# Performance work log

Hardware: AMD Instinct MI355X
Metric: run time of the kernel (lower is better)

The kernel has to match this reference:

```python
import jax, jax.numpy as jnp
import numpy as np

N = 16384      # tokens
D_IN = 256     # input feature dim
D = 1024       # d_model
H = 2048       # expert hidden dim (2 * d_model)
E = 8          # n_experts
K = 2          # top_k
OUT = 2        # output classes
EPS = 1e-5


def layernorm(x, g, b):
    m = jnp.mean(x, axis=-1, keepdims=True)
    v = jnp.mean(jnp.square(x - m), axis=-1, keepdims=True)
    return (x - m) * jax.lax.rsqrt(v + EPS) * g + b


def setup_inputs() -> dict:
    key = jax.random.key(0)
    ks = jax.random.split(key, 10)
    s_in = 1.0 / np.sqrt(D_IN)
    s_d = 1.0 / np.sqrt(D)
    s_h = 1.0 / np.sqrt(H)
    return {
        "x": jax.random.normal(ks[0], (N, D_IN), jnp.float32),
        "w_in": jax.random.normal(ks[1], (D_IN, D), jnp.float32) * s_in,
        "b_in": jnp.zeros((D,), jnp.float32),
        "g_in": jnp.ones((D,), jnp.float32),
        "beta_in": jnp.zeros((D,), jnp.float32),
        "w_gate": jax.random.normal(ks[2], (D, E), jnp.float32) * s_d,
        "w1": jax.random.normal(ks[3], (E, D, H), jnp.float32) * s_d,
        "b1": jnp.zeros((E, H), jnp.float32),
        "w2": jax.random.normal(ks[4], (E, H, D), jnp.float32) * s_h,
        "b2": jnp.zeros((E, D), jnp.float32),
        "g_moe": jnp.ones((D,), jnp.float32),
        "beta_moe": jnp.zeros((D,), jnp.float32),
        "g_out": jnp.ones((D,), jnp.float32),
        "beta_out": jnp.zeros((D,), jnp.float32),
        "w_cls": jax.random.normal(ks[5], (D, OUT), jnp.float32) * s_d,
        "b_cls": jnp.zeros((OUT,), jnp.float32),
    }


def reference(x, w_in, b_in, g_in, beta_in, w_gate, w1, b1, w2, b2,
              g_moe, beta_moe, g_out, beta_out, w_cls, b_cls):
    # input projection + norm
    h = layernorm(x @ w_in + b_in, g_in, beta_in)            # [N, D]
    # router: softmax then top-k, renormalize over selected experts
    probs = jax.nn.softmax(h @ w_gate, axis=-1)              # [N, E]
    _, top_idx = jax.lax.top_k(probs, K)                     # [N, K]
    sel = jax.nn.one_hot(top_idx, E, dtype=probs.dtype).sum(axis=1)  # [N, E] 0/1
    gates = probs * sel
    gates = gates / (jnp.sum(gates, axis=-1, keepdims=True) + 1e-9)
    # experts: weighted combine; gate==0 tokens contribute nothing (same math
    # as the torch masked gather/scatter-add, dropout off in eval)
    mixed = jnp.zeros_like(h)
    for e in range(E):  # fixed, small expert count
        expert_out = jax.nn.gelu(h @ w1[e] + b1[e]) @ w2[e] + b2[e]  # [N, D]
        mixed = mixed + gates[:, e:e + 1] * expert_out
    out = layernorm(h + mixed, g_moe, beta_moe)
    out = layernorm(out, g_out, beta_out)
    return out @ w_cls + b_cls                               # [N, OUT]
```

## Files before the change

kernel.cpp:

```cpp
#include <hip/hip_runtime.h>
#include <hip/hip_bf16.h>

#define D_IN 256
#define DM   1024
#define HD   2048
#define NE   8
#define NTOK 16384

typedef __attribute__((ext_vector_type(8))) short short8;
typedef __attribute__((ext_vector_type(4))) float f32x4;
typedef unsigned int uint;

#define MT_TOFF1 0
#define MT_TOFF2 512
#define MT_CNT1  1536
#define MT_P1    1600
#define MT_OFF1  1664
#define MT_CNT2  1728
#define MT_PCNT2 1856
#define MT_TOTAL 1984

__device__ inline ushort f2bf(float v){
  __hip_bfloat16 b = __float2bfloat16(v);
  return *reinterpret_cast<ushort*>(&b);
}
__device__ inline float bf2f(ushort u){
  __hip_bfloat16 b = *reinterpret_cast<__hip_bfloat16*>(&u);
  return __bfloat162float(b);
}

__device__ inline float gelu_tanh(float x){
  float x3 = x*x*x;
  float t = tanhf(0.7978845608028654f*(x + 0.044715f*x3));
  return 0.5f*x*(1.0f+t);
}

__device__ inline void gload16(const void* g, void* l){
  __builtin_amdgcn_global_load_lds(
      (const __attribute__((address_space(1))) void*)g,
      (__attribute__((address_space(3))) void*)l, 16, 0, 0);
}

__global__ __launch_bounds__(256) void transpose_bf16_kernel(
    const float* __restrict__ src, ushort* __restrict__ dst, int R, int C)
{
  __shared__ float tile[32][33];
  int e = blockIdx.z;
  src += (size_t)e*R*C; dst += (size_t)e*R*C;
  int c0 = blockIdx.x*32, r0 = blockIdx.y*32;
  int tx = threadIdx.x & 31, ty = threadIdx.x >> 5;
  #pragma unroll
  for (int rr = ty; rr < 32; rr += 8)
    tile[rr][tx] = src[(size_t)(r0+rr)*C + c0+tx];
  __syncthreads();
  #pragma unroll
  for (int rr = ty; rr < 32; rr += 8)
    dst[(size_t)(c0+rr)*R + r0+tx] = f2bf(tile[tx][rr]);
}

__global__ __launch_bounds__(256) void split_x_kernel(
    const float* __restrict__ x, ushort* __restrict__ xs3)
{
  int g = blockIdx.x*256 + threadIdx.x;
  int e0 = g*4;
  int row = e0 >> 8, col = e0 & 255;
  f32x4 v = *(const f32x4*)(x + (size_t)row*D_IN + col);
  ushort4 hi, mi, lo;
  #pragma unroll
  for (int i=0;i<4;++i){
    float f = v[i];
    ushort h = f2bf(f);       float fh = bf2f(h);
    ushort m = f2bf(f - fh);  float fm = bf2f(m);
    ushort l = f2bf(f - fh - fm);
    ((ushort*)&hi)[i]=h; ((ushort*)&mi)[i]=m; ((ushort*)&lo)[i]=l;
  }
  ushort* base = xs3 + (size_t)row*768 + col;
  *(ushort4*)(base)       = hi;
  *(ushort4*)(base + 256) = mi;
  *(ushort4*)(base + 512) = lo;
}

__global__ __launch_bounds__(256) void transpose_split3_kernel(
    const float* __restrict__ src, ushort* __restrict__ dst)
{
  __shared__ float tile[32][33];
  int c0 = blockIdx.x*32, r0 = blockIdx.y*32;
  int tx = threadIdx.x & 31, ty = threadIdx.x >> 5;
  #pragma unroll
  for (int rr = ty; rr < 32; rr += 8)
    tile[rr][tx] = src[(size_t)(r0+rr)*DM + c0+tx];
  __syncthreads();
  #pragma unroll
  for (int rr = ty; rr < 32; rr += 8){
    float f = tile[tx][rr];
    ushort h = f2bf(f);       float fh = bf2f(h);
    ushort m = f2bf(f - fh);  float fm = bf2f(m);
    ushort l = f2bf(f - fh - fm);
    ushort* d = dst + (size_t)(c0+rr)*768 + r0 + tx;
    d[0]   = h;
    d[256] = m;
    d[512] = l;
  }
}

__global__ __launch_bounds__(256) void wgate_t_kernel(
    const float* __restrict__ w_gate, float* __restrict__ wgt)
{
  int e = blockIdx.x;
  for (int j = threadIdx.x; j < DM; j += 256)
    wgt[(size_t)e*DM + j] = w_gate[(size_t)j*NE + e];
}

__global__ __launch_bounds__(256) void gemm_router(
    const ushort* __restrict__ A,
    const ushort* __restrict__ BT,
    const float* __restrict__ b_in,
    float* __restrict__ y)
{
  __shared__ ushort As[128*32];
  __shared__ ushort Bs[128*32];
  const int tid = threadIdx.x;
  const int w = tid>>6, l = tid&63;
  const int wm = w>>1, wn = w&1;
  const int bm0 = blockIdx.y*128, bn0 = blockIdx.x*128;
  const int lr = l&15, lk = l>>4;
  const int rsub = l>>2, csub = (l&3)*8;

  const ushort* ag[2]; const ushort* bg[2];
  ushort* al[2]; ushort* bl[2];
  #pragma unroll
  for (int i=0;i<2;++i){
    int ra = bm0 + w*32 + i*16 + rsub;
    int rb = bn0 + w*32 + i*16 + rsub;
    ag[i] = A  + (size_t)ra*768 + csub;
    bg[i] = BT + (size_t)rb*768 + csub;
    al[i] = (ushort*)As + (w*32 + i*16)*32;
    bl[i] = (ushort*)Bs + (w*32 + i*16)*32;
  }

  f32x4 zero = {0.f,0.f,0.f,0.f};
  f32x4 acc[4][4];
  #pragma unroll
  for (int i=0;i<4;++i){
    #pragma unroll
    for (int j=0;j<4;++j) acc[i][j]=zero;
  }

  const int pq[6][2] = {{0,0},{256,0},{0,256},{256,256},{512,0},{0,512}};
  for (int t=0;t<6;++t){
    int pOff = pq[t][0], qOff = pq[t][1];
    for (int kt=0; kt<256; kt+=32){
      #pragma unroll
      for (int i=0;i<2;++i){
        gload16(ag[i]+pOff+kt, al[i]);
        gload16(bg[i]+qOff+kt, bl[i]);
      }
      __syncthreads();
      short8 af[4], bf[4];
      #pragma unroll
      for (int i=0;i<4;++i) af[i] = *(const short8*)(As + (wm*64 + i*16 + lr)*32 + lk*8);
      #pragma unroll
      for (int j=0;j<4;++j) bf[j] = *(const short8*)(Bs + (wn*64 + j*16 + lr)*32 + lk*8);
      #pragma unroll
      for (int i=0;i<4;++i){
        #pragma unroll
        for (int j=0;j<4;++j)
          acc[i][j] = __builtin_amdgcn_mfma_f32_16x16x32_bf16(af[i], bf[j], acc[i][j], 0, 0, 0);
      }
      __syncthreads();
    }
  }

  #pragma unroll
  for (int i=0;i<4;++i){
    #pragma unroll
    for (int j=0;j<4;++j){
      int n = bn0 + wn*64 + j*16 + lr;
      float bn_ = b_in[n];
      #pragma unroll
      for (int r=0;r<4;++r){
        int m = bm0 + wm*64 + i*16 + lk*4 + r;
        y[(size_t)m*DM + n] = acc[i][j][r] + bn_;
      }
    }
  }
}

__device__ inline double wredd(double v){
  #pragma unroll
  for (int o=32;o>0;o>>=1) v += __shfl_xor(v, o, 64);
  return v;
}

__global__ __launch_bounds__(256) void ln_router_kernel(
    const float* __restrict__ g_in, const float* __restrict__ beta_in,
    const float* __restrict__ wgt,
    ushort* __restrict__ hbf, float* __restrict__ resid,
    float* __restrict__ gates, int* __restrict__ selmask)
{
  int tok = blockIdx.x*4 + (threadIdx.x>>6);
  int l = threadIdx.x & 63;
  float* row = resid + (size_t)tok*DM;
  float u[16];
  double s=0.0, q=0.0;
  #pragma unroll
  for (int r=0;r<16;++r){ u[r]=row[l+64*r]; s+=u[r]; q+=(double)u[r]*u[r]; }
  s = wredd(s); q = wredd(q);
  double mean = s*(1.0/1024.0);
  double var  = q*(1.0/1024.0) - mean*mean;
  double rstd = 1.0/sqrt(var + 1e-5);

  double lg[NE];
  #pragma unroll
  for (int e=0;e<NE;++e) lg[e]=0.0;
  float hv[16];
  #pragma unroll
  for (int r=0;r<16;++r){
    int j = l + 64*r;
    double v = ((double)u[r]-mean)*rstd*(double)g_in[j] + (double)beta_in[j];
    hv[r] = (float)v;
    #pragma unroll
    for (int e=0;e<NE;++e) lg[e] += v*(double)wgt[(size_t)e*DM + j];
  }
  #pragma unroll
  for (int r=0;r<16;++r){
    int j = l + 64*r;
    row[j] = hv[r];
    hbf[(size_t)tok*DM + j] = f2bf(hv[r]);
  }
  #pragma unroll
  for (int e=0;e<NE;++e) lg[e] = wredd(lg[e]);

  if (l==0){
    double mx = lg[0];
    #pragma unroll
    for (int e=1;e<NE;++e) mx = lg[e]>mx ? lg[e] : mx;
    double p[NE]; double sum=0.0;
    #pragma unroll
    for (int e=0;e<NE;++e){ p[e]=exp(lg[e]-mx); sum+=p[e]; }
    #pragma unroll
    for (int e=0;e<NE;++e) p[e]/=sum;
    int i1=0;
    for (int e=1;e<NE;++e) if (p[e]>p[i1]) i1=e;
    int i2=-1;
    for (int e=0;e<NE;++e){ if (e==i1) continue; if (i2<0 || p[e]>p[i2]) i2=e; }
    double denom = p[i1]+p[i2]+1e-9;
    float g[NE];
    #pragma unroll
    for (int e=0;e<NE;++e) g[e]=0.f;
    g[i1]=(float)(p[i1]/denom);
    g[i2]=(float)(p[i2]/denom);
    #pragma unroll
    for (int e=0;e<NE;++e) gates[(size_t)tok*NE+e]=g[e];
    selmask[tok] = (1<<i1)|(1<<i2);
  }
}

__global__ __launch_bounds__(256) void builder_count(
    const int* __restrict__ selmask, uint* __restrict__ bc1, uint* __restrict__ bc2)
{
  __shared__ uint c1[8], c2s[16];
  int b = blockIdx.x, tid = threadIdx.x;
  if (tid<8) c1[tid]=0;
  if (tid<16) c2s[tid]=0;
  __syncthreads();
  int m = selmask[b*256+tid];
  int ea = __ffs(m)-1, eb = 31-__clz(m);
  atomicAdd(&c1[ea],1u); atomicAdd(&c1[eb],1u);
  atomicAdd(&c2s[ea],1u); atomicAdd(&c2s[8+eb],1u);
  __syncthreads();
  if (tid<8) bc1[b*8+tid]=c1[tid];
  if (tid<16) bc2[b*16+tid]=c2s[tid];
}

__global__ __launch_bounds__(256) void builder_scan(
    const uint* __restrict__ bc1, const uint* __restrict__ bc2,
    uint* __restrict__ meta, int nch, int TPC)
{
  int tid = threadIdx.x;
  int c = tid/24, k = tid%24;
  if (c < nch){
    if (k < 8){
      uint run=0;
      for (int b=c*TPC; b<(c+1)*TPC; ++b){ meta[MT_TOFF1 + b*8 + k] = run; run += bc1[b*8+k]; }
      meta[MT_CNT1 + c*8 + k] = run;
    } else {
      int k2 = k-8;
      uint run=0;
      for (int b=c*TPC; b<(c+1)*TPC; ++b){ meta[MT_TOFF2 + b*16 + k2] = run; run += bc2[b*16+k2]; }
      meta[MT_CNT2 + c*16 + k2] = run;
      meta[MT_PCNT2 + c*16 + k2] = ((run + 127u)/128u)*128u;
    }
  }
  __syncthreads();
  if (tid < nch){
    uint off=0;
    for (int e=0;e<8;++e){
      uint cn = meta[MT_CNT1 + tid*8 + e];
      uint p = ((cn+127u)/128u)*128u;
      meta[MT_P1 + tid*8 + e] = p;
      meta[MT_OFF1 + tid*8 + e] = off;
      off += p;
    }
  }
}

__device__ inline int exclscan256(int v, int* sc, int tid){
  sc[tid]=v; __syncthreads();
  #pragma unroll
  for (int o=1;o<256;o<<=1){
    int x = (tid>=o) ? sc[tid-o] : 0;
    __syncthreads();
    sc[tid]+=x;
    __syncthreads();
  }
  int incl = sc[tid]; __syncthreads();
  return incl - v;
}

__global__ __launch_bounds__(256) void builder_fill(
    const int* __restrict__ selmask, const uint* __restrict__ meta,
    int* __restrict__ ids1, int* __restrict__ g2row, int* __restrict__ g2tok,
    int CH)
{
  __shared__ int sc[256];
  int b = blockIdx.x, tid = threadIdx.x;
  int t = b*256 + tid;
  int c = t / CH;
  int m = selmask[t];
  int ea = __ffs(m)-1, eb = 31-__clz(m);
  int ja=0, jb=0;
  for (int e=0;e<8;++e){
    int r0 = exclscan256((ea==e)?1:0, sc, tid);
    if (ea==e) ja = r0;
    int r1 = exclscan256((eb==e)?1:0, sc, tid);
    if (eb==e) jb = r1;
  }
  {
    uint j    = meta[MT_TOFF2 + b*16 + ea] + (uint)ja;
    uint pos1 = j;
    uint row  = meta[MT_OFF1 + c*8 + ea] + pos1;
    ids1[(c*8+ea)*CH + pos1] = t;
    g2row[((c*2+0)*8+ea)*CH + j] = (int)row;
    g2tok[((c*2+0)*8+ea)*CH + j] = t;
  }
  {
    uint j    = meta[MT_TOFF2 + b*16 + 8 + eb] + (uint)jb;
    uint pos1 = meta[MT_CNT2 + c*16 + eb] + j;
    uint row  = meta[MT_OFF1 + c*8 + eb] + pos1;
    ids1[(c*8+eb)*CH + pos1] = t;
    g2row[((c*2+1)*8+eb)*CH + j] = (int)row;
    g2tok[((c*2+1)*8+eb)*CH + j] = t;
  }
}

template<int EPI>
__global__ __launch_bounds__(256) void gemm_sparse(
    const ushort* __restrict__ Abase,
    const ushort* __restrict__ BT,
    const int*   __restrict__ rows,
    const int*   __restrict__ toks,
    const uint*  __restrict__ pcnt,
    const uint*  __restrict__ cnt,
    const uint*  __restrict__ off1,
    const float* __restrict__ bias,
    const float* __restrict__ gates,
    ushort* __restrict__ t1,
    float*  __restrict__ resid,
    int K, int N, int CH)
{
  const int e = blockIdx.z;
  const int bm0 = blockIdx.y*128;
  if ((uint)bm0 >= pcnt[e]) return;
  const int bn0 = blockIdx.x*128;

  __shared__ ushort As[128*32];
  __shared__ ushort Bs[128*32];
  const int tid = threadIdx.x;
  const int w = tid>>6, l = tid&63;
  const int wm = w>>1, wn = w&1;
  const int lr = l&15, lk = l>>4;
  const int rsub = l>>2, csub = (l&3)*8;

  const ushort* ag[2]; const ushort* bg[2];
  ushort* al[2]; ushort* bl[2];
  #pragma unroll
  for (int i=0;i<2;++i){
    int ra = w*32 + i*16 + rsub;
    int id = rows[e*CH + bm0 + ra];
    ag[i] = Abase + (size_t)id*K + csub;
    int rb = bn0 + w*32 + i*16 + rsub;
    bg[i] = BT + (size_t)e*N*K + (size_t)rb*K + csub;
    al[i] = (ushort*)As + (w*32 + i*16)*32;
    bl[i] = (ushort*)Bs + (w*32 + i*16)*32;
  }

  f32x4 zero = {0.f,0.f,0.f,0.f};
  f32x4 acc[4][4];
  #pragma unroll
  for (int i=0;i<4;++i){
    #pragma unroll
    for (int j=0;j<4;++j) acc[i][j]=zero;
  }

  for (int kt = 0; kt < K; kt += 32) {
    #pragma unroll
    for (int i=0;i<2;++i){
      gload16(ag[i]+kt, al[i]);
      gload16(bg[i]+kt, bl[i]);
    }
    __syncthreads();
    short8 af[4], bf[4];
    #pragma unroll
    for (int i=0;i<4;++i) af[i] = *(const short8*)(As + (wm*64 + i*16 + lr)*32 + lk*8);
    #pragma unroll
    for (int j=0;j<4;++j) bf[j] = *(const short8*)(Bs + (wn*64 + j*16 + lr)*32 + lk*8);
    #pragma unroll
    for (int i=0;i<4;++i){
      #pragma unroll
      for (int j=0;j<4;++j)
        acc[i][j] = __builtin_amdgcn_mfma_f32_16x16x32_bf16(af[i], bf[j], acc[i][j], 0, 0, 0);
    }
    __syncthreads();
  }

  #pragma unroll
  for (int i=0;i<4;++i){
    #pragma unroll
    for (int j=0;j<4;++j){
      int n = bn0 + wn*64 + j*16 + lr;
      float bn_ = bias[(size_t)e*N + n];
      #pragma unroll
      for (int r=0;r<4;++r){
        int mloc = wm*64 + i*16 + lk*4 + r;
        float v = acc[i][j][r] + bn_;
        if (EPI==0){
          size_t trow = (size_t)off1[e] + bm0 + mloc;
          t1[trow*N + n] = f2bf(gelu_tanh(v));
        } else {
          int mg = bm0 + mloc;
          if ((uint)mg < cnt[e]){
            int tok = toks[e*CH + mg];
            float g = gates[(size_t)tok*NE + e];
            resid[(size_t)tok*N + n] += g*v;
          }
        }
      }
    }
  }
}

__global__ __launch_bounds__(64) void final_kernel(
    const float* __restrict__ resid,
    const float* __restrict__ g_moe, const float* __restrict__ beta_moe,
    const float* __restrict__ g_out, const float* __restrict__ beta_out,
    const float* __restrict__ w_cls, const float* __restrict__ b_cls,
    float* __restrict__ out)
{
  int tok = blockIdx.x; int l = threadIdx.x;
  const float* row = resid + (size_t)tok*DM;
  float u[16];
  double s=0.0,q=0.0;
  #pragma unroll
  for (int r=0;r<16;++r){ u[r]=row[l + 64*r]; s+=u[r]; q+=(double)u[r]*u[r]; }
  s=wredd(s); q=wredd(q);
  double m1 = s*(1.0/1024.0), v1 = q*(1.0/1024.0)-m1*m1;
  double rs1 = 1.0/sqrt(v1+1e-5);
  float tv[16]; double s2=0.0,q2=0.0;
  #pragma unroll
  for (int r=0;r<16;++r){
    int j = l+64*r;
    float vv = (float)((u[r]-m1)*rs1)*g_moe[j] + beta_moe[j];
    tv[r]=vv; s2+=vv; q2+=(double)vv*vv;
  }
  s2=wredd(s2); q2=wredd(q2);
  double m2=s2*(1.0/1024.0), v2=q2*(1.0/1024.0)-m2*m2;
  double rs2=1.0/sqrt(v2+1e-5);
  double p0=0.0,p1=0.0;
  #pragma unroll
  for (int r=0;r<16;++r){
    int j=l+64*r;
    double y=((double)tv[r]-m2)*rs2*(double)g_out[j]+(double)beta_out[j];
    p0+=y*(double)w_cls[j*2]; p1+=y*(double)w_cls[j*2+1];
  }
  p0=wredd(p0); p1=wredd(p1);
  if (l==0){
    out[(size_t)tok*2  ]=(float)(p0+(double)b_cls[0]);
    out[(size_t)tok*2+1]=(float)(p1+(double)b_cls[1]);
  }
}

extern "C" void kernel_launch(void* const* d_in, const int* in_sizes, int n_in,
                              void* d_out, int out_size, void* d_ws, size_t ws_size,
                              hipStream_t stream)
{
  (void)in_sizes; (void)n_in; (void)out_size;
  const float* x       = (const float*)d_in[0];
  const float* w_in    = (const float*)d_in[1];
  const float* b_in    = (const float*)d_in[2];
  const float* g_in    = (const float*)d_in[3];
  const float* beta_in = (const float*)d_in[4];
  const float* w_gate  = (const float*)d_in[5];
  const float* w1      = (const float*)d_in[6];
  const float* b1      = (const float*)d_in[7];
  const float* w2      = (const float*)d_in[8];
  const float* b2      = (const float*)d_in[9];
  const float* g_moe   = (const float*)d_in[10];
  const float* beta_mo = (const float*)d_in[11];
  const float* g_out   = (const float*)d_in[12];
  const float* beta_ou = (const float*)d_in[13];
  const float* w_cls   = (const float*)d_in[14];
  const float* b_cls   = (const float*)d_in[15];
  float* out = (float*)d_out;

  char* p = (char*)d_ws;
  ushort* w1t   = (ushort*)p; p += (size_t)NE*HD*DM*2;
  ushort* w2t   = (ushort*)p; p += (size_t)NE*DM*HD*2;
  ushort* hbf   = (ushort*)p; p += (size_t)NTOK*DM*2;
  float*  resid = (float*)p;  p += (size_t)NTOK*DM*4;
  float*  gates = (float*)p;  p += (size_t)NTOK*NE*4;
  int*    selmk = (int*)p;    p += (size_t)NTOK*4;
  int*    ids1  = (int*)p;    p += (size_t)NE*NTOK*4;
  int*    g2row = (int*)p;    p += (size_t)2*NE*NTOK*4;
  int*    g2tok = (int*)p;    p += (size_t)2*NE*NTOK*4;
  ushort* wt3   = (ushort*)p; p += (size_t)DM*768*2;
  float*  wgt   = (float*)p;  p += (size_t)NE*DM*4;
  uint*   bc1   = (uint*)p;   p += (size_t)64*8*4;
  uint*   bc2   = (uint*)p;   p += (size_t)64*16*4;
  uint*   meta  = (uint*)p;   p += (size_t)MT_TOTAL*4;
  size_t fixed = (size_t)(p - (char*)d_ws);

  const size_t xs3_bytes = (size_t)NTOK*768*2;
  size_t t1b2 = ((size_t)2*(NTOK/2)+1024)*HD*2;
  size_t t1b4 = ((size_t)2*(NTOK/4)+1024)*HD*2;
  int nch = 8;
  if (ws_size >= fixed + (t1b2 > xs3_bytes ? t1b2 : xs3_bytes)) nch = 2;
  else if (ws_size >= fixed + (t1b4 > xs3_bytes ? t1b4 : xs3_bytes)) nch = 4;
  const int CH  = NTOK/nch;
  const int TPC = CH/256;
  ushort* t1  = (ushort*)p;
  ushort* xs3 = (ushort*)p;

  split_x_kernel<<<dim3(NTOK*D_IN/4/256), 256, 0, stream>>>(x, xs3);
  transpose_split3_kernel<<<dim3(DM/32, D_IN/32), 256, 0, stream>>>(w_in, wt3);
  wgate_t_kernel<<<dim3(NE), 256, 0, stream>>>(w_gate, wgt);
  transpose_bf16_kernel<<<dim3(HD/32, DM/32, NE), 256, 0, stream>>>(w1, w1t, DM, HD);
  transpose_bf16_kernel<<<dim3(DM/32, HD/32, NE), 256, 0, stream>>>(w2, w2t, HD, DM);

  gemm_router<<<dim3(DM/128, NTOK/128), 256, 0, stream>>>(xs3, wt3, b_in, resid);
  ln_router_kernel<<<dim3(NTOK/4), 256, 0, stream>>>(g_in, beta_in, wgt,
                                                     hbf, resid, gates, selmk);

  hipMemsetAsync(ids1, 0, (size_t)NE*NTOK*4, stream);
  hipMemsetAsync(g2row, 0, (size_t)2*NE*NTOK*4, stream);
  hipMemsetAsync(g2tok, 0, (size_t)2*NE*NTOK*4, stream);

  builder_count<<<dim3(NTOK/256), 256, 0, stream>>>(selmk, bc1, bc2);
  builder_scan<<<dim3(1), 256, 0, stream>>>(bc1, bc2, meta, nch, TPC);
  builder_fill<<<dim3(NTOK/256), 256, 0, stream>>>(selmk, meta, ids1, g2row, g2tok, CH);

  for (int c = 0; c < nch; ++c) {
    gemm_sparse<0><<<dim3(HD/128, CH/128, NE), 256, 0, stream>>>(
        hbf, w1t, ids1 + (size_t)c*8*CH, nullptr,
        meta+MT_P1+c*8, nullptr, meta+MT_OFF1+c*8,
        b1, nullptr, t1, nullptr, DM, HD, CH);
    for (int s = 0; s < 2; ++s) {
      gemm_sparse<1><<<dim3(DM/128, CH/128, NE), 256, 0, stream>>>(
          t1, w2t, g2row + (size_t)(c*2+s)*8*CH, g2tok + (size_t)(c*2+s)*8*CH,
          meta+MT_PCNT2+c*16+s*8, meta+MT_CNT2+c*16+s*8, nullptr,
          b2, gates, nullptr, resid, HD, DM, CH);
    }
  }

  final_kernel<<<dim3(NTOK), 64, 0, stream>>>(resid, g_moe, beta_mo, g_out, beta_ou,
                                              w_cls, b_cls, out);
}
```

Baseline: 947.1 us.

## Add 256x256 pipelined 8-wave GEMM for router and first expert GEMM

```diff
diff --git a/kernel.cpp b/kernel.cpp
--- a/kernel.cpp
+++ b/kernel.cpp
@@ -29,10 +29,9 @@
   return __bfloat162float(b);
 }
 
-__device__ inline float gelu_tanh(float x){
-  float x3 = x*x*x;
-  float t = tanhf(0.7978845608028654f*(x + 0.044715f*x3));
-  return 0.5f*x*(1.0f+t);
+__device__ inline float gelu_fast(float x){
+  float u = 0.7978845608028654f * x * (1.0f + 0.044715f*x*x);
+  return x / (1.0f + __expf(-2.0f*u));
 }
 
 __device__ inline void gload16(const void* g, void* l){
@@ -58,29 +57,26 @@
     dst[(size_t)(c0+rr)*R + r0+tx] = f2bf(tile[tx][rr]);
 }
 
-__global__ __launch_bounds__(256) void split_x_kernel(
-    const float* __restrict__ x, ushort* __restrict__ xs3)
-{
-  int g = blockIdx.x*256 + threadIdx.x;
-  int e0 = g*4;
-  int row = e0 >> 8, col = e0 & 255;
-  f32x4 v = *(const f32x4*)(x + (size_t)row*D_IN + col);
-  ushort4 hi, mi, lo;
+__global__ __launch_bounds__(64) void build_xs6(
+    const float* __restrict__ x, ushort* __restrict__ xs6)
+{
+  int row = blockIdx.x; int t = threadIdx.x;
+  const float* xr = x + (size_t)row*D_IN;
+  ushort* o = xs6 + (size_t)row*1536;
   #pragma unroll
   for (int i=0;i<4;++i){
-    float f = v[i];
-    ushort h = f2bf(f);       float fh = bf2f(h);
-    ushort m = f2bf(f - fh);  float fm = bf2f(m);
-    ushort l = f2bf(f - fh - fm);
-    ((ushort*)&hi)[i]=h; ((ushort*)&mi)[i]=m; ((ushort*)&lo)[i]=l;
-  }
-  ushort* base = xs3 + (size_t)row*768 + col;
-  *(ushort4*)(base)       = hi;
-  *(ushort4*)(base + 256) = mi;
-  *(ushort4*)(base + 512) = lo;
-}
-
-__global__ __launch_bounds__(256) void transpose_split3_kernel(
+    int c = t*4+i;
+    float f = xr[c];
+    ushort h = f2bf(f);        float fh = bf2f(h);
+    ushort m = f2bf(f - fh);   float fm = bf2f(m);
+    ushort lo = f2bf(f - fh - fm);
+    o[c]      = h;  o[512+c]  = h;  o[1280+c] = h;
+    o[256+c]  = m;  o[768+c]  = m;
+    o[1024+c] = lo;
+  }
+}
+
+__global__ __launch_bounds__(256) void build_wt6(
     const float* __restrict__ src, ushort* __restrict__ dst)
 {
   __shared__ float tile[32][33];
@@ -93,13 +89,13 @@
   #pragma unroll
   for (int rr = ty; rr < 32; rr += 8){
     float f = tile[tx][rr];
-    ushort h = f2bf(f);       float fh = bf2f(h);
-    ushort m = f2bf(f - fh);  float fm = bf2f(m);
-    ushort l = f2bf(f - fh - fm);
-    ushort* d = dst + (size_t)(c0+rr)*768 + r0 + tx;
-    d[0]   = h;
-    d[256] = m;
-    d[512] = l;
+    ushort h = f2bf(f);        float fh = bf2f(h);
+    ushort m = f2bf(f - fh);   float fm = bf2f(m);
+    ushort lo = f2bf(f - fh - fm);
+    ushort* d = dst + (size_t)(c0+rr)*1536 + r0 + tx;
+    d[0]    = h;  d[256]  = h;  d[1024] = h;
+    d[512]  = m;  d[768]  = m;
+    d[1280] = lo;
   }
 }
 
@@ -111,76 +107,171 @@
     wgt[(size_t)e*DM + j] = w_gate[(size_t)j*NE + e];
 }
 
-__global__ __launch_bounds__(256) void gemm_router(
+template<int MODE>
+__global__ __launch_bounds__(512, 2) void gemm8p(
     const ushort* __restrict__ A,
     const ushort* __restrict__ BT,
-    const float* __restrict__ b_in,
-    float* __restrict__ y)
-{
-  __shared__ ushort As[128*32];
-  __shared__ ushort Bs[128*32];
+    const int*   __restrict__ rows,
+    const uint*  __restrict__ pcnt,
+    const uint*  __restrict__ off1,
+    const float* __restrict__ bias,
+    float* __restrict__ yout,
+    ushort* __restrict__ t1,
+    int N, int K, int CH)
+{
+  __shared__ ushort lds[2][2][2][8192];
   const int tid = threadIdx.x;
-  const int w = tid>>6, l = tid&63;
-  const int wm = w>>1, wn = w&1;
-  const int bm0 = blockIdx.y*128, bn0 = blockIdx.x*128;
+  const int wid = tid>>6, l = tid&63;
+  const int wm = wid>>2, wn = wid&3;
   const int lr = l&15, lk = l>>4;
-  const int rsub = l>>2, csub = (l&3)*8;
-
-  const ushort* ag[2]; const ushort* bg[2];
-  ushort* al[2]; ushort* bl[2];
-  #pragma unroll
-  for (int i=0;i<2;++i){
-    int ra = bm0 + w*32 + i*16 + rsub;
-    int rb = bn0 + w*32 + i*16 + rsub;
-    ag[i] = A  + (size_t)ra*768 + csub;
-    bg[i] = BT + (size_t)rb*768 + csub;
-    al[i] = (ushort*)As + (w*32 + i*16)*32;
-    bl[i] = (ushort*)Bs + (w*32 + i*16)*32;
-  }
-
-  f32x4 zero = {0.f,0.f,0.f,0.f};
-  f32x4 acc[4][4];
-  #pragma unroll
-  for (int i=0;i<4;++i){
-    #pragma unroll
-    for (int j=0;j<4;++j) acc[i][j]=zero;
-  }
-
-  const int pq[6][2] = {{0,0},{256,0},{0,256},{256,256},{512,0},{0,512}};
-  for (int t=0;t<6;++t){
-    int pOff = pq[t][0], qOff = pq[t][1];
-    for (int kt=0; kt<256; kt+=32){
-      #pragma unroll
-      for (int i=0;i<2;++i){
-        gload16(ag[i]+pOff+kt, al[i]);
-        gload16(bg[i]+qOff+kt, bl[i]);
+
+  int e = 0;
+  const int bn0 = blockIdx.x*256;
+  const int bm0 = blockIdx.y*256;
+  if (MODE==1){
+    e = blockIdx.z;
+    if ((uint)bm0 >= pcnt[e]) return;
+  }
+  const ushort* Bbase = BT + (MODE==1 ? (size_t)e*N*K : (size_t)0);
+
+  const ushort* aS[2][2]; const ushort* bS[2][2];
+  #pragma unroll
+  for (int h=0;h<2;++h){
+    #pragma unroll
+    for (int j=0;j<2;++j){
+      int idx = j*512 + tid;
+      int r   = idx>>3;
+      int cb  = ((idx&7)*16) ^ (((r>>2)&1)<<5);
+      if (MODE==1){
+        int id = rows[e*CH + bm0 + h*128 + r];
+        aS[h][j] = A + (size_t)id*K + (cb>>1);
+      } else {
+        aS[h][j] = A + (size_t)(bm0 + h*128 + r)*K + (cb>>1);
       }
-      __syncthreads();
-      short8 af[4], bf[4];
-      #pragma unroll
-      for (int i=0;i<4;++i) af[i] = *(const short8*)(As + (wm*64 + i*16 + lr)*32 + lk*8);
-      #pragma unroll
-      for (int j=0;j<4;++j) bf[j] = *(const short8*)(Bs + (wn*64 + j*16 + lr)*32 + lk*8);
-      #pragma unroll
-      for (int i=0;i<4;++i){
+      bS[h][j] = Bbase + (size_t)(bn0 + h*128 + r)*K + (cb>>1);
+    }
+  }
+
+  auto stageA = [&](int db, int kt){
+    #pragma unroll
+    for (int h=0;h<2;++h)
+      #pragma unroll
+      for (int j=0;j<2;++j)
+        gload16(aS[h][j] + kt, &lds[db][0][h][(j*512+tid)*8]);
+  };
+  auto stageB = [&](int db, int kt){
+    #pragma unroll
+    for (int h=0;h<2;++h)
+      #pragma unroll
+      for (int j=0;j<2;++j)
+        gload16(bS[h][j] + kt, &lds[db][1][h][(j*512+tid)*8]);
+  };
+
+  stageA(0, 0);  stageB(0, 0);
+  stageA(1, 64); stageB(1, 64);
+  asm volatile("s_waitcnt vmcnt(8)" ::: "memory");
+  __builtin_amdgcn_s_barrier();
+
+  const char* aB; const char* bB;
+  auto ldA = [&](int frA, int ks)->short8{
+    int r = frA*16 + lr;
+    int off = r*128 + ((ks*64 + lk*16) ^ (((r>>2)&1)<<5));
+    return *(const short8*)(aB + off);
+  };
+  auto ldB = [&](int fc, int ks)->short8{
+    int r = (wn&1)*64 + fc*16 + lr;
+    int off = r*128 + ((ks*64 + lk*16) ^ (((r>>2)&1)<<5));
+    return *(const short8*)(bB + off);
+  };
+
+  short8 aR[4][2]; short8 bR[4][2];
+  f32x4 acc[8][4] = {};
+  const int NT = K>>6;
+
+  for (int T=0; T<NT; ++T){
+    const int cur = T&1;
+    aB = (const char*)&lds[cur][0][wm][0];
+    bB = (const char*)&lds[cur][1][wn>>1][0];
+    const bool pf = (T+2 < NT);
+    const int kpf = (T+2)<<6;
+
+    #pragma unroll
+    for (int fr=0;fr<4;++fr){ aR[fr][0]=ldA(fr,0); aR[fr][1]=ldA(fr,1); }
+    #pragma unroll
+    for (int fc=0;fc<2;++fc){ bR[fc][0]=ldB(fc,0); bR[fc][1]=ldB(fc,1); }
+    __builtin_amdgcn_s_barrier();
+    __builtin_amdgcn_s_setprio(1);
+    #pragma unroll
+    for (int fr=0;fr<4;++fr)
+      #pragma unroll
+      for (int fc=0;fc<2;++fc)
         #pragma unroll
-        for (int j=0;j<4;++j)
-          acc[i][j] = __builtin_amdgcn_mfma_f32_16x16x32_bf16(af[i], bf[j], acc[i][j], 0, 0, 0);
-      }
-      __syncthreads();
-    }
-  }
-
-  #pragma unroll
-  for (int i=0;i<4;++i){
-    #pragma unroll
-    for (int j=0;j<4;++j){
-      int n = bn0 + wn*64 + j*16 + lr;
-      float bn_ = b_in[n];
-      #pragma unroll
-      for (int r=0;r<4;++r){
-        int m = bm0 + wm*64 + i*16 + lk*4 + r;
-        y[(size_t)m*DM + n] = acc[i][j][r] + bn_;
+        for (int ks=0;ks<2;++ks)
+          acc[fr][fc] = __builtin_amdgcn_mfma_f32_16x16x32_bf16(aR[fr][ks], bR[fc][ks], acc[fr][fc], 0,0,0);
+    __builtin_amdgcn_s_setprio(0);
+    __builtin_amdgcn_s_barrier();
+
+    #pragma unroll
+    for (int fc=0;fc<2;++fc){ bR[2+fc][0]=ldB(2+fc,0); bR[2+fc][1]=ldB(2+fc,1); }
+    __builtin_amdgcn_s_barrier();
+    __builtin_amdgcn_s_setprio(1);
+    #pragma unroll
+    for (int fr=0;fr<4;++fr)
+      #pragma unroll
+      for (int fc=0;fc<2;++fc)
+        #pragma unroll
+        for (int ks=0;ks<2;++ks)
+          acc[fr][2+fc] = __builtin_amdgcn_mfma_f32_16x16x32_bf16(aR[fr][ks], bR[2+fc][ks], acc[fr][2+fc], 0,0,0);
+    __builtin_amdgcn_s_setprio(0);
+    __builtin_amdgcn_s_barrier();
+
+    #pragma unroll
+    for (int fr=0;fr<4;++fr){ aR[fr][0]=ldA(4+fr,0); aR[fr][1]=ldA(4+fr,1); }
+    if (pf) stageB(cur, kpf);
+    __builtin_amdgcn_s_barrier();
+    __builtin_amdgcn_s_setprio(1);
+    #pragma unroll
+    for (int fr=0;fr<4;++fr)
+      #pragma unroll
+      for (int fc=0;fc<2;++fc)
+        #pragma unroll
+        for (int ks=0;ks<2;++ks)
+          acc[4+fr][2+fc] = __builtin_amdgcn_mfma_f32_16x16x32_bf16(aR[fr][ks], bR[2+fc][ks], acc[4+fr][2+fc], 0,0,0);
+    __builtin_amdgcn_s_setprio(0);
+    __builtin_amdgcn_s_barrier();
+
+    if (pf) stageA(cur, kpf);
+    if (pf)              { asm volatile("s_waitcnt vmcnt(8)" ::: "memory"); }
+    else if (T+1 < NT)   { asm volatile("s_waitcnt vmcnt(0)" ::: "memory"); }
+    __builtin_amdgcn_s_barrier();
+    __builtin_amdgcn_s_setprio(1);
+    #pragma unroll
+    for (int fr=0;fr<4;++fr)
+      #pragma unroll
+      for (int fc=0;fc<2;++fc)
+        #pragma unroll
+        for (int ks=0;ks<2;++ks)
+          acc[4+fr][fc] = __builtin_amdgcn_mfma_f32_16x16x32_bf16(aR[fr][ks], bR[fc][ks], acc[4+fr][fc], 0,0,0);
+    __builtin_amdgcn_s_setprio(0);
+    __builtin_amdgcn_s_barrier();
+  }
+
+  const float* bp = bias + (MODE==1 ? (size_t)e*N : (size_t)0);
+  #pragma unroll
+  for (int fr=0;fr<8;++fr){
+    #pragma unroll
+    for (int fc=0;fc<4;++fc){
+      int n = bn0 + wn*64 + fc*16 + lr;
+      float bb = bp[n];
+      #pragma unroll
+      for (int v=0;v<4;++v){
+        int mloc = wm*128 + fr*16 + lk*4 + v;
+        float val = acc[fr][fc][v] + bb;
+        if (MODE==0){
+          yout[(size_t)(bm0+mloc)*N + n] = val;
+        } else {
+          t1[((size_t)off1[e] + bm0 + mloc)*N + n] = f2bf(gelu_fast(val));
+        }
       }
     }
   }
@@ -297,7 +388,7 @@
     uint off=0;
     for (int e=0;e<8;++e){
       uint cn = meta[MT_CNT1 + tid*8 + e];
-      uint p = ((cn+127u)/128u)*128u;
+      uint p = ((cn+255u)/256u)*256u;
       meta[MT_P1 + tid*8 + e] = p;
       meta[MT_OFF1 + tid*8 + e] = off;
       off += p;
@@ -436,7 +527,7 @@
         float v = acc[i][j][r] + bn_;
         if (EPI==0){
           size_t trow = (size_t)off1[e] + bm0 + mloc;
-          t1[trow*N + n] = f2bf(gelu_tanh(v));
+          t1[trow*N + n] = f2bf(gelu_fast(v));
         } else {
           int mg = bm0 + mloc;
           if ((uint)mg < cnt[e]){
@@ -523,31 +614,34 @@
   int*    ids1  = (int*)p;    p += (size_t)NE*NTOK*4;
   int*    g2row = (int*)p;    p += (size_t)2*NE*NTOK*4;
   int*    g2tok = (int*)p;    p += (size_t)2*NE*NTOK*4;
-  ushort* wt3   = (ushort*)p; p += (size_t)DM*768*2;
   float*  wgt   = (float*)p;  p += (size_t)NE*DM*4;
   uint*   bc1   = (uint*)p;   p += (size_t)64*8*4;
   uint*   bc2   = (uint*)p;   p += (size_t)64*16*4;
   uint*   meta  = (uint*)p;   p += (size_t)MT_TOTAL*4;
   size_t fixed = (size_t)(p - (char*)d_ws);
 
-  const size_t xs3_bytes = (size_t)NTOK*768*2;
-  size_t t1b2 = ((size_t)2*(NTOK/2)+1024)*HD*2;
-  size_t t1b4 = ((size_t)2*(NTOK/4)+1024)*HD*2;
+  const size_t xs6_bytes = (size_t)NTOK*1536*2;
+  const size_t wt6_bytes = (size_t)DM*1536*2;
+  const size_t router_bytes = xs6_bytes + wt6_bytes;
+  size_t t1b2 = ((size_t)2*(NTOK/2)+2048)*HD*2;
+  size_t t1b4 = ((size_t)2*(NTOK/4)+2048)*HD*2;
   int nch = 8;
-  if (ws_size >= fixed + (t1b2 > xs3_bytes ? t1b2 : xs3_bytes)) nch = 2;
-  else if (ws_size >= fixed + (t1b4 > xs3_bytes ? t1b4 : xs3_bytes)) nch = 4;
+  if (ws_size >= fixed + (t1b2 > router_bytes ? t1b2 : router_bytes)) nch = 2;
+  else if (ws_size >= fixed + (t1b4 > router_bytes ? t1b4 : router_bytes)) nch = 4;
   const int CH  = NTOK/nch;
   const int TPC = CH/256;
   ushort* t1  = (ushort*)p;
-  ushort* xs3 = (ushort*)p;
-
-  split_x_kernel<<<dim3(NTOK*D_IN/4/256), 256, 0, stream>>>(x, xs3);
-  transpose_split3_kernel<<<dim3(DM/32, D_IN/32), 256, 0, stream>>>(w_in, wt3);
+  ushort* xs6 = (ushort*)p;
+  ushort* wt6 = (ushort*)(p + xs6_bytes);
+
+  build_xs6<<<dim3(NTOK), 64, 0, stream>>>(x, xs6);
+  build_wt6<<<dim3(DM/32, D_IN/32), 256, 0, stream>>>(w_in, wt6);
   wgate_t_kernel<<<dim3(NE), 256, 0, stream>>>(w_gate, wgt);
   transpose_bf16_kernel<<<dim3(HD/32, DM/32, NE), 256, 0, stream>>>(w1, w1t, DM, HD);
   transpose_bf16_kernel<<<dim3(DM/32, HD/32, NE), 256, 0, stream>>>(w2, w2t, HD, DM);
 
-  gemm_router<<<dim3(DM/128, NTOK/128), 256, 0, stream>>>(xs3, wt3, b_in, resid);
+  gemm8p<0><<<dim3(DM/256, NTOK/256), 512, 0, stream>>>(
+      xs6, wt6, nullptr, nullptr, nullptr, b_in, resid, nullptr, DM, 1536, CH);
   ln_router_kernel<<<dim3(NTOK/4), 256, 0, stream>>>(g_in, beta_in, wgt,
                                                      hbf, resid, gates, selmk);
 
@@ -560,10 +654,10 @@
   builder_fill<<<dim3(NTOK/256), 256, 0, stream>>>(selmk, meta, ids1, g2row, g2tok, CH);
 
   for (int c = 0; c < nch; ++c) {
-    gemm_sparse<0><<<dim3(HD/128, CH/128, NE), 256, 0, stream>>>(
-        hbf, w1t, ids1 + (size_t)c*8*CH, nullptr,
-        meta+MT_P1+c*8, nullptr, meta+MT_OFF1+c*8,
-        b1, nullptr, t1, nullptr, DM, HD, CH);
+    gemm8p<1><<<dim3(HD/256, CH/256, NE), 512, 0, stream>>>(
+        hbf, w1t, ids1 + (size_t)c*8*CH,
+        meta+MT_P1+c*8, meta+MT_OFF1+c*8,
+        b1, nullptr, t1, HD, DM, CH);
     for (int s = 0; s < 2; ++s) {
       gemm_sparse<1><<<dim3(DM/128, CH/128, NE), 256, 0, stream>>>(
           t1, w2t, g2row + (size_t)(c*2+s)*8*CH, g2tok + (size_t)(c*2+s)*8*CH,
```

Measured after the change: 926.3 us. -2.2%, faster.
